# Kernel optimization log

Hardware: AMD Instinct MI355X
Metric: run time of the kernel (lower is better)

Reference implementation:

```python
import math
import jax, jax.numpy as jnp
import numpy as np

B, T, C = 4, 2048, 1024
NH = 16
HD = C // NH  # 64

def setup_inputs() -> dict:
    key = jax.random.key(0)
    k1, k2, k3 = jax.random.split(key, 3)
    x = jax.random.normal(k1, (B, T, C), dtype=jnp.float32)
    # init scale ~ 1/sqrt(fan_in) to keep activations sane
    W_attn = jax.random.normal(k2, (C, 3 * C), dtype=jnp.float32) * (1.0 / math.sqrt(C))
    b_attn = jnp.zeros((3 * C,), dtype=jnp.float32)
    W_proj = jax.random.normal(k3, (C, C), dtype=jnp.float32) * (1.0 / math.sqrt(C))
    b_proj = jnp.zeros((C,), dtype=jnp.float32)
    return {"x": x, "W_attn": W_attn, "b_attn": b_attn, "W_proj": W_proj, "b_proj": b_proj}

def reference(x, W_attn, b_attn, W_proj, b_proj):
    b, t, c = x.shape
    qkv = x @ W_attn + b_attn                      # [B,T,3C]
    q, k, v = jnp.split(qkv, 3, axis=-1)           # each [B,T,C]
    # [B,T,C] -> [B,NH,T,HD]
    def heads(z):
        return z.reshape(b, t, NH, HD).transpose(0, 2, 1, 3)
    q, k, v = heads(q), heads(k), heads(v)
    scale = 1.0 / math.sqrt(HD)
    att = jnp.einsum('bhqd,bhkd->bhqk', q, k) * scale   # [B,NH,T,T]
    causal = jnp.tril(jnp.ones((t, t), dtype=bool))      # [T,T]
    att = jnp.where(causal[None, None, :, :], att, -jnp.inf)
    att = jax.nn.softmax(att, axis=-1)
    # dropout p=0.0 -> identity
    y = jnp.einsum('bhqk,bhkd->bhqd', att, v)            # [B,NH,T,HD]
    y = y.transpose(0, 2, 1, 3).reshape(b, t, c)         # [B,T,C]
    return y @ W_proj + b_proj
```

## Files before the change

kernel.cpp:

```cpp
#include <hip/hip_runtime.h>
#include <hip/hip_bf16.h>


typedef __bf16 bf16;
typedef __bf16 bf16x4 __attribute__((ext_vector_type(4)));
typedef __bf16 bf16x8 __attribute__((ext_vector_type(8)));
typedef float  f32x4  __attribute__((ext_vector_type(4)));

#define MFMA16(a, b, c) __builtin_amdgcn_mfma_f32_16x16x32_bf16((a), (b), (c), 0, 0, 0)

#define GLOAD16(g, l)                                                 \
    __builtin_amdgcn_global_load_lds(                                 \
        (const __attribute__((address_space(1))) void*)(g),           \
        (__attribute__((address_space(3))) void*)(l), 16, 0, 0)

static constexpr int Bsz = 4;
static constexpr int T   = 2048;
static constexpr int Cc  = 1024;
static constexpr int NH  = 16;
static constexpr int HD  = 64;
static constexpr int C3  = 3 * Cc;

__global__ void prep(const float* __restrict__ x, bf16* __restrict__ xb,
                     const float* __restrict__ W_attn, bf16* __restrict__ WtA) {
    const int bid = blockIdx.x;
    const int tid = threadIdx.x;
    if (bid < 4096) {
        size_t i = ((size_t)bid * 256 + tid) * 8;
        f32x4 a0 = *(const f32x4*)(x + i);
        f32x4 a1 = *(const f32x4*)(x + i + 4);
        bf16x8 v;
#pragma unroll
        for (int e = 0; e < 4; ++e) { v[e] = (bf16)a0[e]; v[e + 4] = (bf16)a1[e]; }
        *(bf16x8*)(xb + i) = v;
    } else {
        __shared__ float tile[32][33];
        const int tb = bid - 4096;
        const int bx = (tb % (C3 / 32)) * 32;
        const int by = (tb / (C3 / 32)) * 32;
        const int tx = tid & 31, ty = tid >> 5;
#pragma unroll
        for (int i = 0; i < 32; i += 8)
            tile[ty + i][tx] = W_attn[(size_t)(by + ty + i) * C3 + bx + tx];
        __syncthreads();
#pragma unroll
        for (int i = 0; i < 32; i += 8)
            WtA[(size_t)(bx + ty + i) * Cc + by + tx] = (bf16)tile[tx][ty + i];
    }
}

__global__ void transpose_f32_bf16(const float* __restrict__ in, bf16* __restrict__ out,
                                   int R, int Ccols) {
    __shared__ float tile[32][33];
    int bx = blockIdx.x * 32;
    int by = blockIdx.y * 32;
    int tx = threadIdx.x, ty = threadIdx.y;
#pragma unroll
    for (int i = 0; i < 32; i += 8)
        tile[ty + i][tx] = in[(size_t)(by + ty + i) * Ccols + bx + tx];
    __syncthreads();
#pragma unroll
    for (int i = 0; i < 32; i += 8)
        out[(size_t)(bx + ty + i) * R + by + tx] = (bf16)tile[tx][ty + i];
}

__global__ __launch_bounds__(512, 4)
void gemm_qkv(const bf16* __restrict__ A, const bf16* __restrict__ Bt,
              const float* __restrict__ bias,
              bf16* __restrict__ qo, bf16* __restrict__ ko, bf16* __restrict__ vt,
              int M, int N, int K) {
    constexpr int BM = 256, BN = 128, BK = 64;
    __shared__ bf16 As[BM * BK];
    __shared__ bf16 Bs[BN * BK];

    const int tid  = threadIdx.x;
    const int wave = tid >> 6, lane = tid & 63;
    const int quad = lane >> 4, l16 = lane & 15;
    const int wm = wave >> 1, wn = wave & 1;
    const int m0 = blockIdx.x * BM, n0 = blockIdx.y * BN;

    f32x4 acc[4][4] = {};

    const int lrow = lane >> 3;
    const int lcol = ((lane & 7) ^ lrow) * 8;
    const bf16* Ab = A  + (size_t)(m0 + wave * 8 + lrow) * K + lcol;
    const bf16* Bb = Bt + (size_t)(n0 + wave * 8 + lrow) * K + lcol;
    const int wofs = wave * 512;
    const int sxo = l16 & 7;

    for (int k0 = 0; k0 < K; k0 += BK) {
#pragma unroll
        for (int r = 0; r < 4; ++r)
            GLOAD16(Ab + (size_t)(r * 64) * K + k0, As + wofs + r * 4096);
#pragma unroll
        for (int r = 0; r < 2; ++r)
            GLOAD16(Bb + (size_t)(r * 64) * K + k0, Bs + wofs + r * 4096);
        __syncthreads();

#pragma unroll
        for (int ks = 0; ks < 2; ++ks) {
            bf16x8 af[4], bfr[4];
#pragma unroll
            for (int i = 0; i < 4; ++i)
                af[i] = *(const bf16x8*)(&As[(wm * 64 + i * 16 + l16) * BK
                                             + (((ks * 4 + quad) ^ sxo) << 3)]);
#pragma unroll
            for (int j = 0; j < 4; ++j)
                bfr[j] = *(const bf16x8*)(&Bs[(wn * 64 + j * 16 + l16) * BK
                                              + (((ks * 4 + quad) ^ sxo) << 3)]);
#pragma unroll
            for (int i = 0; i < 4; ++i)
#pragma unroll
                for (int j = 0; j < 4; ++j)
                    acc[i][j] = MFMA16(af[i], bfr[j], acc[i][j]);
        }
        __syncthreads();
    }

    const int which = n0 >> 10;
    const int nc0 = n0 & 1023;
    if (which < 2) {
        bf16* dst = which ? ko : qo;
#pragma unroll
        for (int j = 0; j < 4; ++j) {
            int colg = n0 + wn * 64 + j * 16 + l16;
            int coll = nc0 + wn * 64 + j * 16 + l16;
            float bv = bias[colg];
#pragma unroll
            for (int i = 0; i < 4; ++i) {
                int rowb = m0 + wm * 64 + i * 16 + quad * 4;
#pragma unroll
                for (int r = 0; r < 4; ++r)
                    dst[(size_t)(rowb + r) * Cc + coll] = (bf16)(acc[i][j][r] + bv);
            }
        }
    } else {
#pragma unroll
        for (int j = 0; j < 4; ++j) {
            int colg = n0 + wn * 64 + j * 16 + l16;
            int coll = nc0 + wn * 64 + j * 16 + l16;
            int h = coll >> 6, d = coll & 63;
            float bv = bias[colg];
            bf16* vhead_d = vt + ((size_t)h * HD + d) * T;
#pragma unroll
            for (int i = 0; i < 4; ++i) {
                int rowb = m0 + wm * 64 + i * 16 + quad * 4;
                int b = rowb >> 11;
                int t = rowb & 2047;
                bf16x4 pk;
#pragma unroll
                for (int r = 0; r < 4; ++r) pk[r] = (bf16)(acc[i][j][r] + bv);
                *(bf16x4*)(vhead_d + (size_t)b * NH * HD * T + t) = pk;
            }
        }
    }
}

__global__ __launch_bounds__(256)
void gemm_bt(const bf16* __restrict__ A, const bf16* __restrict__ Bt,
             const float* __restrict__ bias, float* __restrict__ C,
             int M, int N, int K) {
    constexpr int BM = 128, BN = 128, BK = 64;
    __shared__ bf16 As[2][BM * BK];
    __shared__ bf16 Bs[2][BN * BK];

    const int tid  = threadIdx.x;
    const int wave = tid >> 6, lane = tid & 63;
    const int quad = lane >> 4, l16 = lane & 15;
    const int wm = wave & 1, wn = wave >> 1;
    const int m0 = blockIdx.x * BM, n0 = blockIdx.y * BN;

    f32x4 acc[4][4] = {};

    const int lrow = lane >> 3;
    const int lcol = (lane & 7) * 8;
    const bf16* Ab = A  + (size_t)(m0 + wave * 8 + lrow) * K + lcol;
    const bf16* Bb = Bt + (size_t)(n0 + wave * 8 + lrow) * K + lcol;
    const int wofs = wave * 512;

#pragma unroll
    for (int r = 0; r < 4; ++r) {
        GLOAD16(Ab + (size_t)r * 32 * K, As[0] + wofs + r * 2048);
        GLOAD16(Bb + (size_t)r * 32 * K, Bs[0] + wofs + r * 2048);
    }

    int cur = 0;
    for (int k0 = 0; k0 < K; k0 += BK) {
        __syncthreads();
        if (k0 + BK < K) {
#pragma unroll
            for (int r = 0; r < 4; ++r) {
                GLOAD16(Ab + (size_t)r * 32 * K + k0 + BK, As[cur ^ 1] + wofs + r * 2048);
                GLOAD16(Bb + (size_t)r * 32 * K + k0 + BK, Bs[cur ^ 1] + wofs + r * 2048);
            }
        }
        const bf16* Asc = As[cur];
        const bf16* Bsc = Bs[cur];
#pragma unroll
        for (int ks = 0; ks < 2; ++ks) {
            bf16x8 af[4], bfr[4];
#pragma unroll
            for (int i = 0; i < 4; ++i)
                af[i] = *(const bf16x8*)(&Asc[(wm * 64 + i * 16 + l16) * BK + ks * 32 + quad * 8]);
#pragma unroll
            for (int j = 0; j < 4; ++j)
                bfr[j] = *(const bf16x8*)(&Bsc[(wn * 64 + j * 16 + l16) * BK + ks * 32 + quad * 8]);
#pragma unroll
            for (int i = 0; i < 4; ++i)
#pragma unroll
                for (int j = 0; j < 4; ++j)
                    acc[i][j] = MFMA16(af[i], bfr[j], acc[i][j]);
        }
        cur ^= 1;
    }

#pragma unroll
    for (int j = 0; j < 4; ++j) {
        int col = n0 + wn * 64 + j * 16 + l16;
        float bv = bias[col];
#pragma unroll
        for (int i = 0; i < 4; ++i) {
            int rowb = m0 + wm * 64 + i * 16 + quad * 4;
#pragma unroll
            for (int r = 0; r < 4; ++r)
                C[(size_t)(rowb + r) * N + col] = acc[i][j][r] + bv;
        }
    }
}

__global__ __launch_bounds__(256, 6)
void attn_fused(const bf16* __restrict__ qb, const bf16* __restrict__ kb,
                const bf16* __restrict__ vtb, bf16* __restrict__ y) {
    constexpr int LKD = 72;
    constexpr int LVT = 40;
    constexpr int LPS = 40;
    __shared__ bf16 Ks[2][32 * LKD];
    __shared__ bf16 Vt[2][64 * LVT];
    __shared__ bf16 Ps[4][16 * LPS];

    const int tid  = threadIdx.x;
    const int wave = tid >> 6, lane = tid & 63;
    const int quad = lane >> 4, l16 = lane & 15;
    const int bid = blockIdx.x;
    const int qt = 31 - (bid >> 6);
    const int hb = bid & 63;
    const int b = hb >> 4, h = hb & 15;
    const int q0 = qt * 64;

    const bf16* qbase  = qb + (size_t)b * T * Cc + h * HD;
    const bf16* kbase  = kb + (size_t)b * T * Cc + h * HD;
    const bf16* vthead = vtb + (size_t)(b * NH + h) * HD * T;
    bf16* yrow = y + (size_t)b * T * Cc + h * HD;

    const int srK = tid >> 3, scK = (tid & 7) * 8;
    const int srV = tid >> 2, scV = (tid & 3) * 8;

    bf16x8 ones;
#pragma unroll
    for (int e = 0; e < 8; ++e) ones[e] = (bf16)1.0f;

    bf16x8 qf[2];
    {
        int qrow = q0 + wave * 16 + l16;
#pragma unroll
        for (int dblk = 0; dblk < 2; ++dblk) {
            bf16x8 v = *(const bf16x8*)(qbase + (size_t)qrow * Cc + dblk * 32 + quad * 8);
#pragma unroll
            for (int e = 0; e < 8; ++e) v[e] = (bf16)((float)v[e] * 0.18033688f);
            qf[dblk] = v;
        }
    }

    f32x4 o[4] = {};
    f32x4 osum = {};

    const int w0 = q0 + wave * 16;
    const int nt = q0 / 32 + 2;

    bf16x8 kp = *(const bf16x8*)(kbase + (size_t)srK * Cc + scK);
    bf16x8 vp = *(const bf16x8*)(vthead + (size_t)srV * T + scV);
    *(bf16x8*)(&Ks[0][srK * LKD + scK]) = kp;
    *(bf16x8*)(&Vt[0][srV * LVT + scV]) = vp;

    int cur = 0;
    for (int it = 0; it < nt; ++it) {
        const int kt = it * 32;
        __syncthreads();

        const bool more = (it + 1 < nt);
        if (more) {
            int ktn = kt + 32;
            kp = *(const bf16x8*)(kbase + (size_t)(ktn + srK) * Cc + scK);
            vp = *(const bf16x8*)(vthead + (size_t)srV * T + ktn + scV);
        }

        const bf16* ksc = Ks[cur];
        const bf16* vtc = Vt[cur];
        if (kt <= w0 + 15) {
            __builtin_amdgcn_s_setprio(1);
            f32x4 st[2] = {};
#pragma unroll
            for (int km = 0; km < 2; ++km) {
                bf16x8 kf0 = *(const bf16x8*)(&ksc[(km * 16 + l16) * LKD + quad * 8]);
                bf16x8 kf1 = *(const bf16x8*)(&ksc[(km * 16 + l16) * LKD + 32 + quad * 8]);
                st[km] = MFMA16(kf0, qf[0], st[km]);
                st[km] = MFMA16(kf1, qf[1], st[km]);
            }

            const bool needmask = (kt + 31 > w0);
            const int qrel = w0 + l16 - kt;
#pragma unroll
            for (int km = 0; km < 2; ++km)
#pragma unroll
                for (int r = 0; r < 4; ++r) {
                    float v = st[km][r];
                    if (needmask) {
                        int key = km * 16 + quad * 4 + r;
                        v = (key <= qrel) ? v : -INFINITY;
                    }
                    st[km][r] = __builtin_exp2f(v);
                }

            bf16* pw = &Ps[wave][0];
#pragma unroll
            for (int km = 0; km < 2; ++km) {
                bf16x4 pk;
#pragma unroll
                for (int r = 0; r < 4; ++r) pk[r] = (bf16)st[km][r];
                *(bf16x4*)(&pw[l16 * LPS + km * 16 + quad * 4]) = pk;
            }
            bf16x8 pf = *(const bf16x8*)(&pw[l16 * LPS + quad * 8]);

#pragma unroll
            for (int dd = 0; dd < 4; ++dd) {
                bf16x8 vf = *(const bf16x8*)(&vtc[(dd * 16 + l16) * LVT + quad * 8]);
                o[dd] = MFMA16(pf, vf, o[dd]);
            }
            osum = MFMA16(pf, ones, osum);
            __builtin_amdgcn_s_setprio(0);
        }

        if (more) {
            *(bf16x8*)(&Ks[cur ^ 1][srK * LKD + scK]) = kp;
            *(bf16x8*)(&Vt[cur ^ 1][srV * LVT + scV]) = vp;
        }
        cur ^= 1;
    }

#pragma unroll
    for (int r = 0; r < 4; ++r) {
        float inv = 1.0f / osum[r];
        int t = w0 + quad * 4 + r;
#pragma unroll
        for (int dd = 0; dd < 4; ++dd)
            yrow[(size_t)t * Cc + dd * 16 + l16] = (bf16)(o[dd][r] * inv);
    }
}

extern "C" void kernel_launch(void* const* d_in, const int* in_sizes, int n_in,
                              void* d_out, int out_size, void* d_ws, size_t ws_size,
                              hipStream_t stream) {
    const float* x      = (const float*)d_in[0];
    const float* W_attn = (const float*)d_in[1];
    const float* b_attn = (const float*)d_in[2];
    const float* W_proj = (const float*)d_in[3];
    const float* b_proj = (const float*)d_in[4];
    float* out = (float*)d_out;

    const int M = Bsz * T;
    const size_t R = (size_t)M * Cc;

    bf16* qb  = (bf16*)d_ws;
    bf16* kb  = qb + R;
    bf16* vtb = kb + R;
    bf16* xb  = vtb + R;
    bf16* yb  = xb;
    bf16* WtA = (bf16*)d_out;
    bf16* WtP = qb;

    prep<<<4096 + 3072, 256, 0, stream>>>(x, xb, W_attn, WtA);
    gemm_qkv<<<dim3(M / 256, C3 / 128), 512, 0, stream>>>(xb, WtA, b_attn, qb, kb, vtb, M, C3, Cc);
    attn_fused<<<2048, 256, 0, stream>>>(qb, kb, vtb, yb);
    transpose_f32_bf16<<<dim3(Cc / 32, Cc / 32), dim3(32, 8), 0, stream>>>(W_proj, WtP, Cc, Cc);
    gemm_bt<<<dim3(M / 128, Cc / 128), 256, 0, stream>>>(yb, WtP, b_proj, out, M, Cc, Cc);
}
```

Measured before the change: 249.2 us.

## Swizzle LDS layouts and use direct global-to-LDS loads in attention and projection GEMM

The projection GEMM moves to 256x128 tiles with 512 threads and a single-buffered LDS tile whose 16-byte chunks are XOR-swizzled by row. It syncs before and after each K step. The attention kernel drops its padded K/V LDS layout for XOR-swizzled unpadded tiles and loads them with global_load_lds instead of register staging. The aim is fewer LDS bank conflicts, less register pressure and less instruction overhead for staging, at the cost of losing double-buffer overlap in the GEMM.

```diff
diff --git a/kernel.cpp b/kernel.cpp
--- a/kernel.cpp
+++ b/kernel.cpp
@@ -156,62 +156,56 @@
     }
 }
 
-__global__ __launch_bounds__(256)
+__global__ __launch_bounds__(512, 4)
 void gemm_bt(const bf16* __restrict__ A, const bf16* __restrict__ Bt,
              const float* __restrict__ bias, float* __restrict__ C,
              int M, int N, int K) {
-    constexpr int BM = 128, BN = 128, BK = 64;
-    __shared__ bf16 As[2][BM * BK];
-    __shared__ bf16 Bs[2][BN * BK];
+    constexpr int BM = 256, BN = 128, BK = 64;
+    __shared__ bf16 As[BM * BK];
+    __shared__ bf16 Bs[BN * BK];
 
     const int tid  = threadIdx.x;
     const int wave = tid >> 6, lane = tid & 63;
     const int quad = lane >> 4, l16 = lane & 15;
-    const int wm = wave & 1, wn = wave >> 1;
+    const int wm = wave >> 1, wn = wave & 1;
     const int m0 = blockIdx.x * BM, n0 = blockIdx.y * BN;
 
     f32x4 acc[4][4] = {};
 
     const int lrow = lane >> 3;
-    const int lcol = (lane & 7) * 8;
+    const int lcol = ((lane & 7) ^ lrow) * 8;
     const bf16* Ab = A  + (size_t)(m0 + wave * 8 + lrow) * K + lcol;
     const bf16* Bb = Bt + (size_t)(n0 + wave * 8 + lrow) * K + lcol;
     const int wofs = wave * 512;
-
-#pragma unroll
-    for (int r = 0; r < 4; ++r) {
-        GLOAD16(Ab + (size_t)r * 32 * K, As[0] + wofs + r * 2048);
-        GLOAD16(Bb + (size_t)r * 32 * K, Bs[0] + wofs + r * 2048);
-    }
-
-    int cur = 0;
+    const int sxo = l16 & 7;
+
     for (int k0 = 0; k0 < K; k0 += BK) {
-        __syncthreads();
-        if (k0 + BK < K) {
-#pragma unroll
-            for (int r = 0; r < 4; ++r) {
-                GLOAD16(Ab + (size_t)r * 32 * K + k0 + BK, As[cur ^ 1] + wofs + r * 2048);
-                GLOAD16(Bb + (size_t)r * 32 * K + k0 + BK, Bs[cur ^ 1] + wofs + r * 2048);
-            }
-        }
-        const bf16* Asc = As[cur];
-        const bf16* Bsc = Bs[cur];
+#pragma unroll
+        for (int r = 0; r < 4; ++r)
+            GLOAD16(Ab + (size_t)(r * 64) * K + k0, As + wofs + r * 4096);
+#pragma unroll
+        for (int r = 0; r < 2; ++r)
+            GLOAD16(Bb + (size_t)(r * 64) * K + k0, Bs + wofs + r * 4096);
+        __syncthreads();
+
 #pragma unroll
         for (int ks = 0; ks < 2; ++ks) {
             bf16x8 af[4], bfr[4];
 #pragma unroll
             for (int i = 0; i < 4; ++i)
-                af[i] = *(const bf16x8*)(&Asc[(wm * 64 + i * 16 + l16) * BK + ks * 32 + quad * 8]);
+                af[i] = *(const bf16x8*)(&As[(wm * 64 + i * 16 + l16) * BK
+                                             + (((ks * 4 + quad) ^ sxo) << 3)]);
 #pragma unroll
             for (int j = 0; j < 4; ++j)
-                bfr[j] = *(const bf16x8*)(&Bsc[(wn * 64 + j * 16 + l16) * BK + ks * 32 + quad * 8]);
+                bfr[j] = *(const bf16x8*)(&Bs[(wn * 64 + j * 16 + l16) * BK
+                                              + (((ks * 4 + quad) ^ sxo) << 3)]);
 #pragma unroll
             for (int i = 0; i < 4; ++i)
 #pragma unroll
                 for (int j = 0; j < 4; ++j)
                     acc[i][j] = MFMA16(af[i], bfr[j], acc[i][j]);
         }
-        cur ^= 1;
+        __syncthreads();
     }
 
 #pragma unroll
@@ -231,11 +225,9 @@
 __global__ __launch_bounds__(256, 6)
 void attn_fused(const bf16* __restrict__ qb, const bf16* __restrict__ kb,
                 const bf16* __restrict__ vtb, bf16* __restrict__ y) {
-    constexpr int LKD = 72;
-    constexpr int LVT = 40;
     constexpr int LPS = 40;
-    __shared__ bf16 Ks[2][32 * LKD];
-    __shared__ bf16 Vt[2][64 * LVT];
+    __shared__ bf16 Ks[2][32 * 64];
+    __shared__ bf16 Vt[2][64 * 32];
     __shared__ bf16 Ps[4][16 * LPS];
 
     const int tid  = threadIdx.x;
@@ -252,8 +244,16 @@
     const bf16* vthead = vtb + (size_t)(b * NH + h) * HD * T;
     bf16* yrow = y + (size_t)b * T * Cc + h * HD;
 
-    const int srK = tid >> 3, scK = (tid & 7) * 8;
-    const int srV = tid >> 2, scV = (tid & 3) * 8;
+    const int krow = lane >> 3;
+    const int kchk = (lane & 7) ^ krow;
+    const bf16* kg = kbase + (size_t)(wave * 8 + krow) * Cc + kchk * 8;
+    const int vrow = lane >> 2;
+    const int vchk = (lane & 3) ^ (vrow & 3);
+    const bf16* vg = vthead + (size_t)(wave * 16 + vrow) * T + vchk * 8;
+    const int wofsK = wave * 512;
+    const int wofsV = wave * 512;
+    const int sxk = l16 & 7;
+    const int sxv = l16 & 3;
 
     bf16x8 ones;
 #pragma unroll
@@ -277,21 +277,17 @@
     const int w0 = q0 + wave * 16;
     const int nt = q0 / 32 + 2;
 
-    bf16x8 kp = *(const bf16x8*)(kbase + (size_t)srK * Cc + scK);
-    bf16x8 vp = *(const bf16x8*)(vthead + (size_t)srV * T + scV);
-    *(bf16x8*)(&Ks[0][srK * LKD + scK]) = kp;
-    *(bf16x8*)(&Vt[0][srV * LVT + scV]) = vp;
+    GLOAD16(kg, &Ks[0][wofsK]);
+    GLOAD16(vg, &Vt[0][wofsV]);
 
     int cur = 0;
     for (int it = 0; it < nt; ++it) {
         const int kt = it * 32;
         __syncthreads();
 
-        const bool more = (it + 1 < nt);
-        if (more) {
-            int ktn = kt + 32;
-            kp = *(const bf16x8*)(kbase + (size_t)(ktn + srK) * Cc + scK);
-            vp = *(const bf16x8*)(vthead + (size_t)srV * T + ktn + scV);
+        if (it + 1 < nt) {
+            GLOAD16(kg + (size_t)(kt + 32) * Cc, &Ks[cur ^ 1][wofsK]);
+            GLOAD16(vg + (kt + 32),              &Vt[cur ^ 1][wofsV]);
         }
 
         const bf16* ksc = Ks[cur];
@@ -301,8 +297,8 @@
             f32x4 st[2] = {};
 #pragma unroll
             for (int km = 0; km < 2; ++km) {
-                bf16x8 kf0 = *(const bf16x8*)(&ksc[(km * 16 + l16) * LKD + quad * 8]);
-                bf16x8 kf1 = *(const bf16x8*)(&ksc[(km * 16 + l16) * LKD + 32 + quad * 8]);
+                bf16x8 kf0 = *(const bf16x8*)(&ksc[(km * 16 + l16) * 64 + ((quad ^ sxk) << 3)]);
+                bf16x8 kf1 = *(const bf16x8*)(&ksc[(km * 16 + l16) * 64 + (((quad + 4) ^ sxk) << 3)]);
                 st[km] = MFMA16(kf0, qf[0], st[km]);
                 st[km] = MFMA16(kf1, qf[1], st[km]);
             }
@@ -333,16 +329,11 @@
 
 #pragma unroll
             for (int dd = 0; dd < 4; ++dd) {
-                bf16x8 vf = *(const bf16x8*)(&vtc[(dd * 16 + l16) * LVT + quad * 8]);
+                bf16x8 vf = *(const bf16x8*)(&vtc[(dd * 16 + l16) * 32 + ((quad ^ sxv) << 3)]);
                 o[dd] = MFMA16(pf, vf, o[dd]);
             }
             osum = MFMA16(pf, ones, osum);
             __builtin_amdgcn_s_setprio(0);
-        }
-
-        if (more) {
-            *(bf16x8*)(&Ks[cur ^ 1][srK * LKD + scK]) = kp;
-            *(bf16x8*)(&Vt[cur ^ 1][srV * LVT + scV]) = vp;
         }
         cur ^= 1;
     }
@@ -382,5 +373,5 @@
     gemm_qkv<<<dim3(M / 256, C3 / 128), 512, 0, stream>>>(xb, WtA, b_attn, qb, kb, vtb, M, C3, Cc);
     attn_fused<<<2048, 256, 0, stream>>>(qb, kb, vtb, yb);
     transpose_f32_bf16<<<dim3(Cc / 32, Cc / 32), dim3(32, 8), 0, stream>>>(W_proj, WtP, Cc, Cc);
-    gemm_bt<<<dim3(M / 128, Cc / 128), 256, 0, stream>>>(yb, WtP, b_proj, out, M, Cc, Cc);
-}
+    gemm_bt<<<dim3(M / 256, Cc / 128), 512, 0, stream>>>(yb, WtP, b_proj, out, M, Cc, Cc);
+}
```

After: 258.4 us. 1.04x slower.

## Load attention K/V tiles directly to LDS with swizzled 64-key double buffer

Applied to the files above, without the earlier changes.

Replaces the register-staged K/V tile loads with global_load_lds direct-to-LDS copies, using an XOR swizzle in place of padded rows to avoid bank conflicts. Each iteration now covers 64 keys as two 32-key sub-tiles, which halves the number of barriers. The larger LDS footprint forces launch bounds down from 6 to 4 blocks per CU, trading occupancy for fewer register round-trips and fewer syncs.

```diff
diff --git a/kernel.cpp b/kernel.cpp
--- a/kernel.cpp
+++ b/kernel.cpp
@@ -228,14 +228,12 @@
     }
 }
 
-__global__ __launch_bounds__(256, 6)
+__global__ __launch_bounds__(256, 4)
 void attn_fused(const bf16* __restrict__ qb, const bf16* __restrict__ kb,
                 const bf16* __restrict__ vtb, bf16* __restrict__ y) {
-    constexpr int LKD = 72;
-    constexpr int LVT = 40;
     constexpr int LPS = 40;
-    __shared__ bf16 Ks[2][32 * LKD];
-    __shared__ bf16 Vt[2][64 * LVT];
+    __shared__ bf16 Ks[2][2][32 * 64];
+    __shared__ bf16 Vt[2][2][64 * 32];
     __shared__ bf16 Ps[4][16 * LPS];
 
     const int tid  = threadIdx.x;
@@ -252,8 +250,16 @@
     const bf16* vthead = vtb + (size_t)(b * NH + h) * HD * T;
     bf16* yrow = y + (size_t)b * T * Cc + h * HD;
 
-    const int srK = tid >> 3, scK = (tid & 7) * 8;
-    const int srV = tid >> 2, scV = (tid & 3) * 8;
+    const int krow = lane >> 3;
+    const int kchk = (lane & 7) ^ krow;
+    const bf16* kg = kbase + (size_t)(wave * 8 + krow) * Cc + kchk * 8;
+    const int vrow = lane >> 2;
+    const int vchk = (lane & 3) ^ (vrow & 3);
+    const bf16* vg = vthead + (size_t)(wave * 16 + vrow) * T + vchk * 8;
+    const int wofsK = wave * 512;
+    const int wofsV = wave * 512;
+    const int sxk = l16 & 7;
+    const int sxv = l16 & 3;
 
     bf16x8 ones;
 #pragma unroll
@@ -275,74 +281,75 @@
     f32x4 osum = {};
 
     const int w0 = q0 + wave * 16;
-    const int nt = q0 / 32 + 2;
-
-    bf16x8 kp = *(const bf16x8*)(kbase + (size_t)srK * Cc + scK);
-    bf16x8 vp = *(const bf16x8*)(vthead + (size_t)srV * T + scV);
-    *(bf16x8*)(&Ks[0][srK * LKD + scK]) = kp;
-    *(bf16x8*)(&Vt[0][srV * LVT + scV]) = vp;
+    const int nt2 = q0 / 64 + 1;
+
+    GLOAD16(kg,            &Ks[0][0][wofsK]);
+    GLOAD16(kg + 32 * Cc,  &Ks[0][1][wofsK]);
+    GLOAD16(vg,            &Vt[0][0][wofsV]);
+    GLOAD16(vg + 32,       &Vt[0][1][wofsV]);
 
     int cur = 0;
-    for (int it = 0; it < nt; ++it) {
-        const int kt = it * 32;
-        __syncthreads();
-
-        const bool more = (it + 1 < nt);
-        if (more) {
-            int ktn = kt + 32;
-            kp = *(const bf16x8*)(kbase + (size_t)(ktn + srK) * Cc + scK);
-            vp = *(const bf16x8*)(vthead + (size_t)srV * T + ktn + scV);
-        }
-
-        const bf16* ksc = Ks[cur];
-        const bf16* vtc = Vt[cur];
-        if (kt <= w0 + 15) {
-            __builtin_amdgcn_s_setprio(1);
-            f32x4 st[2] = {};
-#pragma unroll
-            for (int km = 0; km < 2; ++km) {
-                bf16x8 kf0 = *(const bf16x8*)(&ksc[(km * 16 + l16) * LKD + quad * 8]);
-                bf16x8 kf1 = *(const bf16x8*)(&ksc[(km * 16 + l16) * LKD + 32 + quad * 8]);
-                st[km] = MFMA16(kf0, qf[0], st[km]);
-                st[km] = MFMA16(kf1, qf[1], st[km]);
+    for (int it = 0; it < nt2; ++it) {
+        const int kt0 = it * 64;
+        __syncthreads();
+
+        if (it + 1 < nt2) {
+            const bf16* kgn = kg + (size_t)(kt0 + 64) * Cc;
+            const bf16* vgn = vg + (kt0 + 64);
+            GLOAD16(kgn,           &Ks[cur ^ 1][0][wofsK]);
+            GLOAD16(kgn + 32 * Cc, &Ks[cur ^ 1][1][wofsK]);
+            GLOAD16(vgn,           &Vt[cur ^ 1][0][wofsV]);
+            GLOAD16(vgn + 32,      &Vt[cur ^ 1][1][wofsV]);
+        }
+
+#pragma unroll
+        for (int s = 0; s < 2; ++s) {
+            const int kt = kt0 + s * 32;
+            if (kt <= w0 + 15) {
+                const bf16* ksc = Ks[cur][s];
+                const bf16* vtc = Vt[cur][s];
+                __builtin_amdgcn_s_setprio(1);
+                f32x4 st[2] = {};
+#pragma unroll
+                for (int km = 0; km < 2; ++km) {
+                    bf16x8 kf0 = *(const bf16x8*)(&ksc[(km * 16 + l16) * 64 + ((quad ^ sxk) << 3)]);
+                    bf16x8 kf1 = *(const bf16x8*)(&ksc[(km * 16 + l16) * 64 + (((quad + 4) ^ sxk) << 3)]);
+                    st[km] = MFMA16(kf0, qf[0], st[km]);
+                    st[km] = MFMA16(kf1, qf[1], st[km]);
+                }
+
+                const bool needmask = (kt + 31 > w0);
+                const int qrel = w0 + l16 - kt;
+#pragma unroll
+                for (int km = 0; km < 2; ++km)
+#pragma unroll
+                    for (int r = 0; r < 4; ++r) {
+                        float v = st[km][r];
+                        if (needmask) {
+                            int key = km * 16 + quad * 4 + r;
+                            v = (key <= qrel) ? v : -INFINITY;
+                        }
+                        st[km][r] = __builtin_exp2f(v);
+                    }
+
+                bf16* pw = &Ps[wave][0];
+#pragma unroll
+                for (int km = 0; km < 2; ++km) {
+                    bf16x4 pk;
+#pragma unroll
+                    for (int r = 0; r < 4; ++r) pk[r] = (bf16)st[km][r];
+                    *(bf16x4*)(&pw[l16 * LPS + km * 16 + quad * 4]) = pk;
+                }
+                bf16x8 pf = *(const bf16x8*)(&pw[l16 * LPS + quad * 8]);
+
+#pragma unroll
+                for (int dd = 0; dd < 4; ++dd) {
+                    bf16x8 vf = *(const bf16x8*)(&vtc[(dd * 16 + l16) * 32 + ((quad ^ sxv) << 3)]);
+                    o[dd] = MFMA16(pf, vf, o[dd]);
+                }
+                osum = MFMA16(pf, ones, osum);
+                __builtin_amdgcn_s_setprio(0);
             }
-
-            const bool needmask = (kt + 31 > w0);
-            const int qrel = w0 + l16 - kt;
-#pragma unroll
-            for (int km = 0; km < 2; ++km)
-#pragma unroll
-                for (int r = 0; r < 4; ++r) {
-                    float v = st[km][r];
-                    if (needmask) {
-                        int key = km * 16 + quad * 4 + r;
-                        v = (key <= qrel) ? v : -INFINITY;
-                    }
-                    st[km][r] = __builtin_exp2f(v);
-                }
-
-            bf16* pw = &Ps[wave][0];
-#pragma unroll
-            for (int km = 0; km < 2; ++km) {
-                bf16x4 pk;
-#pragma unroll
-                for (int r = 0; r < 4; ++r) pk[r] = (bf16)st[km][r];
-                *(bf16x4*)(&pw[l16 * LPS + km * 16 + quad * 4]) = pk;
-            }
-            bf16x8 pf = *(const bf16x8*)(&pw[l16 * LPS + quad * 8]);
-
-#pragma unroll
-            for (int dd = 0; dd < 4; ++dd) {
-                bf16x8 vf = *(const bf16x8*)(&vtc[(dd * 16 + l16) * LVT + quad * 8]);
-                o[dd] = MFMA16(pf, vf, o[dd]);
-            }
-            osum = MFMA16(pf, ones, osum);
-            __builtin_amdgcn_s_setprio(0);
-        }
-
-        if (more) {
-            *(bf16x8*)(&Ks[cur ^ 1][srK * LKD + scK]) = kp;
-            *(bf16x8*)(&Vt[cur ^ 1][srV * LVT + scV]) = vp;
         }
         cur ^= 1;
     }
```

Result: slower. 265.7 us (+6.6%).
